# Kernel tuning notes

Measured on AMD Instinct MI355X. Metric: run time of the kernel, lower is better.

The kernel has to match this reference:

```python
import jax, jax.numpy as jnp
import numpy as np

N, D_IN, WID, LAT, DPD, H, N_SEG = 131072, 128, 512, 512, 128, 8, 256


def cumulative_segment_mean(data, segment_ids):
    # prefix mean that resets at each new (sorted) segment id
    n = data.shape[0]
    idx = jnp.arange(n)
    seg_start = jnp.concatenate([jnp.ones((1,), bool), segment_ids[1:] != segment_ids[:-1]])
    # index of the first element of each token's segment
    start_idx = jax.lax.associative_scan(jnp.maximum, jnp.where(seg_start, idx, 0))
    cs = jnp.cumsum(data, axis=0)
    base = jnp.where((start_idx > 0)[:, None], cs[jnp.maximum(start_idx - 1, 0)], jnp.zeros((), data.dtype))
    count = (idx - start_idx + 1).astype(data.dtype)[:, None]
    return (cs - base) / count


def setup_inputs() -> dict:
    key = jax.random.key(0)
    ks = jax.random.split(key, 12)
    he = lambda k, sh: jax.random.normal(k, sh, jnp.float32) * np.sqrt(2.0 / sh[0]).astype(np.float32)
    inputs = jax.random.normal(ks[0], (N, D_IN), jnp.float32)
    segment_ids = jnp.sort(jax.random.randint(ks[1], (N,), 0, N_SEG, dtype=jnp.int64))
    return {
        "inputs": inputs,
        "segment_ids": segment_ids,
        "W1": he(ks[2], (D_IN, WID)), "b1": jnp.zeros((WID,), jnp.float32),
        "W2": he(ks[3], (WID, WID)), "b2": jnp.zeros((WID,), jnp.float32),
        "W3": he(ks[4], (WID, LAT)), "b3": jnp.zeros((LAT,), jnp.float32),
        "Wr": he(ks[5], (LAT, LAT)), "br": jnp.zeros((LAT,), jnp.float32),
        "W_k": he(ks[6], (LAT + D_IN, DPD * H)),
        "W_q": jax.random.normal(ks[7], (H, DPD), jnp.float32) * 0.05,
    }


def reference(inputs, segment_ids, W1, b1, W2, b2, W3, b3, Wr, br, W_k, W_q):
    relu = jax.nn.relu
    h = relu(inputs @ W1 + b1)          # psi layer 1
    h = relu(h @ W2 + b2)               # psi layer 2
    encoded = relu(h @ W3 + b3)         # psi latent projection
    agg = cumulative_segment_mean(encoded, segment_ids)
    agg = relu(agg @ Wr + br)           # rho
    combined = jnp.concatenate([inputs, agg], axis=-1)   # [N, D_IN+LAT]
    keys = (combined @ W_k).reshape(inputs.shape[0], H, DPD)  # split+stack heads
    preattn = jnp.einsum('nhd,hd->nh', keys, W_q) / jnp.sqrt(jnp.float32(DPD))
    return preattn
```

## Files before the change

kernel.cpp:

```cpp
#include <hip/hip_runtime.h>
#include <hip/hip_bf16.h>
#include <stdint.h>

typedef unsigned short ushortT;
typedef __bf16 bf16x8 __attribute__((ext_vector_type(8)));
typedef float f32x4 __attribute__((ext_vector_type(4)));

#define N_TOK 131072
#define NSEG  256
#define RSPL  8

__device__ __forceinline__ uint32_t f2bf(float f) {
  union { float f; uint32_t u; } c; c.f = f;
  uint32_t u = c.u;
  u += 0x7fffu + ((u >> 16) & 1u);
  return u >> 16;
}
__device__ __forceinline__ float bf2f(uint32_t b) {
  union { uint32_t u; float f; } c; c.u = b << 16;
  return c.f;
}

__device__ __forceinline__ void gload_lds16(const void* g, void* l) {
  __builtin_amdgcn_global_load_lds(
      (const __attribute__((address_space(1))) void*)g,
      (__attribute__((address_space(3))) void*)l, 16, 0, 0);
}


__global__ void transpose_bf16_kernel(const float* __restrict__ W, ushortT* __restrict__ WT,
                                      int Kd, int Nd) {
  int i = blockIdx.x * 256 + threadIdx.x;
  if (i < Kd * Nd) {
    int n = i / Kd, k = i % Kd;
    WT[i] = (ushortT)f2bf(W[(size_t)k * Nd + n]);
  }
}

__global__ void weff_kernel(const float* __restrict__ Wk, const float* __restrict__ Wq,
                            ushortT* __restrict__ weffT) {
  const int c = blockIdx.x;
  const int lane = threadIdx.x;
  const float rs = 0.08838834764831845f;
#pragma unroll
  for (int h = 0; h < 8; ++h) {
    float acc = Wk[(size_t)c * 1024 + h * 128 + lane] * Wq[h * 128 + lane]
              + Wk[(size_t)c * 1024 + h * 128 + 64 + lane] * Wq[h * 128 + 64 + lane];
#pragma unroll
    for (int off = 32; off >= 1; off >>= 1) acc += __shfl_xor(acc, off, 64);
    if (lane == 0) {
      weffT[h * 640 + c]       = (ushortT)f2bf(acc * rs);
      weffT[(h + 8) * 640 + c] = 0;
    }
  }
}

__global__ void seg_bounds_kernel(const int* __restrict__ seg, int* __restrict__ gbnd) {
  const int s = (int)threadIdx.x + (int)blockIdx.x * 512;
  if (s > NSEG) return;
  int lo = 0, hi = N_TOK;
  while (lo < hi) { int m = (lo + hi) >> 1; if (seg[m] < s) lo = m + 1; else hi = m; }
  gbnd[s] = lo;
}


template <int K, bool RELU, bool BIAS, bool XF32>
__global__ __launch_bounds__(256, 2)
void gemm_m97_kernel(const void* __restrict__ Av, const ushortT* __restrict__ BT,
                     const float* __restrict__ bias, ushortT* __restrict__ C) {
  __shared__ ushortT lA[128 * 64];
  __shared__ ushortT lB[128 * 64];
  constexpr int NT = K / 64;

  const int nwg  = (int)gridDim.x;
  const int cpx  = nwg >> 3;
  const int flat = (int)blockIdx.x;
  const int swz  = (flat & 7) * cpx + (flat >> 3);
  const int bm   = swz >> 2;
  const int bn   = swz & 3;

  const int t = (int)threadIdx.x;
  const int w = t >> 6, lane = t & 63;
  const int wm = w >> 1, wn = w & 1;
  const int q = lane >> 4, lr = lane & 15;

  const int srow = t >> 3;
  const int slc  = (t & 7) ^ (srow & 7);

  const ushortT* Ab = nullptr;
  const float*   Xf = nullptr;
  if (XF32) Xf = (const float*)Av + (size_t)(bm * 128 + srow) * 128 + slc * 8;
  else      Ab = (const ushortT*)Av + (size_t)(bm * 128 + srow) * K + slc * 8;
  const ushortT* Bg = BT + (size_t)(bn * 128 + srow) * K + slc * 8;

  f32x4 acc[4][4];
#pragma unroll
  for (int i = 0; i < 4; ++i)
#pragma unroll
    for (int j = 0; j < 4; ++j) acc[i][j] = 0.f;

  const int cc0 = (q ^ (lr & 7)) << 4;
  const int cc1 = ((4 + q) ^ (lr & 7)) << 4;
  const char* lAc = (const char*)lA;
  const char* lBc = (const char*)lB;

#pragma unroll 1
  for (int kt = 0; kt < NT; ++kt) {
    if (XF32) {
      const float* src = Xf + kt * 64;
#pragma unroll
      for (int j = 0; j < 4; ++j) {
        const float4 v0 = *(const float4*)(src + (size_t)j * 32 * 128);
        const float4 v1 = *(const float4*)(src + (size_t)j * 32 * 128 + 4);
        uint4 pk;
        pk.x = f2bf(v0.x) | (f2bf(v0.y) << 16);
        pk.y = f2bf(v0.z) | (f2bf(v0.w) << 16);
        pk.z = f2bf(v1.x) | (f2bf(v1.y) << 16);
        pk.w = f2bf(v1.z) | (f2bf(v1.w) << 16);
        *(uint4*)((char*)lA + j * 4096 + t * 16) = pk;
      }
    } else {
      const ushortT* src = Ab + kt * 64;
#pragma unroll
      for (int j = 0; j < 4; ++j)
        gload_lds16(src + (size_t)j * 32 * K, (char*)lA + j * 4096 + t * 16);
    }
    {
      const ushortT* src = Bg + kt * 64;
#pragma unroll
      for (int j = 0; j < 4; ++j)
        gload_lds16(src + (size_t)j * 32 * K, (char*)lB + j * 4096 + t * 16);
    }
    __syncthreads();

    bf16x8 a0[4], a1[4], b0[4], b1[4];
#pragma unroll
    for (int m = 0; m < 4; ++m) {
      const int ro = (wm * 64 + m * 16 + lr) * 128;
      a0[m] = *(const bf16x8*)(lAc + ro + cc0);
      a1[m] = *(const bf16x8*)(lAc + ro + cc1);
    }
#pragma unroll
    for (int n = 0; n < 4; ++n) {
      const int ro = (wn * 64 + n * 16 + lr) * 128;
      b0[n] = *(const bf16x8*)(lBc + ro + cc0);
      b1[n] = *(const bf16x8*)(lBc + ro + cc1);
    }

    __builtin_amdgcn_s_setprio(1);
#pragma unroll
    for (int n = 0; n < 4; ++n)
#pragma unroll
      for (int m = 0; m < 4; ++m)
        acc[m][n] = __builtin_amdgcn_mfma_f32_16x16x32_bf16(a0[m], b0[n], acc[m][n], 0, 0, 0);
#pragma unroll
    for (int n = 0; n < 4; ++n)
#pragma unroll
      for (int m = 0; m < 4; ++m)
        acc[m][n] = __builtin_amdgcn_mfma_f32_16x16x32_bf16(a1[m], b1[n], acc[m][n], 0, 0, 0);
    __builtin_amdgcn_s_setprio(0);

    __syncthreads();
  }

  const int row0 = bm * 128 + wm * 64 + q * 4;
  const int col0 = bn * 128 + wn * 64 + lr;
#pragma unroll
  for (int n = 0; n < 4; ++n) {
    const int col = col0 + n * 16;
    const float bvv = BIAS ? bias[col] : 0.f;
#pragma unroll
    for (int m = 0; m < 4; ++m) {
#pragma unroll
      for (int r = 0; r < 4; ++r) {
        float v = acc[m][n][r] + bvv;
        if (RELU) v = fmaxf(v, 0.f);
        C[(size_t)(row0 + m * 16 + r) * 512 + col] = (ushortT)f2bf(v);
      }
    }
  }
}


__global__ __launch_bounds__(256)
void seg_sum_kernel(const ushortT* __restrict__ z, const int* __restrict__ gbnd,
                    float* __restrict__ part, int c0, int rows) {
  const int s  = (int)blockIdx.x >> 3;
  const int rg = (int)blockIdx.x & 7;
  const int t  = (int)threadIdx.x;

  const int gb0 = gbnd[s], gb1 = gbnd[s + 1];
  int beg = gb0 > c0 ? gb0 : c0;
  int end = gb1 < c0 + rows ? gb1 : c0 + rows;
  int len = end - beg; if (len < 0) len = 0;
  const int r0 = beg + ((len * rg) >> 3);
  const int r1 = beg + ((len * (rg + 1)) >> 3);

  float a0 = 0.f, a1 = 0.f;
  const uint32_t* __restrict__ zp = (const uint32_t*)z;
  int r = r0;
  for (; r + 8 <= r1; r += 8) {
    uint32_t v[8];
#pragma unroll
    for (int i = 0; i < 8; ++i) v[i] = zp[(size_t)(r + i - c0) * 256 + t];
#pragma unroll
    for (int i = 0; i < 8; ++i) { a0 += bf2f(v[i] & 0xffffu); a1 += bf2f(v[i] >> 16); }
  }
  for (; r < r1; ++r) {
    const uint32_t v = zp[(size_t)(r - c0) * 256 + t];
    a0 += bf2f(v & 0xffffu); a1 += bf2f(v >> 16);
  }
  float2 pv; pv.x = a0; pv.y = a1;
  ((float2*)part)[(s * 8 + rg) * 256 + t] = pv;
}

__global__ __launch_bounds__(256)
void seg_scan2_kernel(const ushortT* __restrict__ z, ushortT* __restrict__ gout,
                      const int* __restrict__ gbnd, const float* __restrict__ br,
                      const float* __restrict__ part,
                      const float* __restrict__ cin, float* __restrict__ cout,
                      int c0, int rows) {
  const int s  = (int)blockIdx.x >> 3;
  const int rg = (int)blockIdx.x & 7;
  const int t  = (int)threadIdx.x;

  const int gb0 = gbnd[s], gb1 = gbnd[s + 1];
  int beg = gb0 > c0 ? gb0 : c0;
  int end = gb1 < c0 + rows ? gb1 : c0 + rows;
  int len = end - beg; if (len < 0) len = 0;
  const int r0 = beg + ((len * rg) >> 3);
  const int r1 = beg + ((len * (rg + 1)) >> 3);

  const float2 cv = ((const float2*)cin)[s * 256 + t];
  float a0 = cv.x, a1 = cv.y;
  for (int q2 = 0; q2 < rg; ++q2) {
    const float2 pv = ((const float2*)part)[(s * 8 + q2) * 256 + t];
    a0 += pv.x; a1 += pv.y;
  }
  int cb = c0 - gb0; if (cb < 0) cb = 0;
  const int seglen = gb1 - gb0; if (cb > seglen) cb = seglen;
  const int cnt0 = cb + (r0 - beg);

  const float b0 = br[2 * t], b1v = br[2 * t + 1];
  const uint32_t* __restrict__ zp = (const uint32_t*)z;
  uint32_t* __restrict__ gp = (uint32_t*)gout;

  int r = r0;
  for (; r + 8 <= r1; r += 8) {
    uint32_t v[8];
#pragma unroll
    for (int i = 0; i < 8; ++i) v[i] = zp[(size_t)(r + i - c0) * 256 + t];
#pragma unroll
    for (int i = 0; i < 8; ++i) {
      a0 += bf2f(v[i] & 0xffffu);
      a1 += bf2f(v[i] >> 16);
      const float inv = 1.0f / (float)(cnt0 + (r + i) - r0 + 1);
      const float g0 = fmaxf(fmaf(a0, inv, b0), 0.f);
      const float g1 = fmaxf(fmaf(a1, inv, b1v), 0.f);
      gp[(size_t)(r + i - c0) * 256 + t] = f2bf(g0) | (f2bf(g1) << 16);
    }
  }
  for (; r < r1; ++r) {
    const uint32_t v = zp[(size_t)(r - c0) * 256 + t];
    a0 += bf2f(v & 0xffffu);
    a1 += bf2f(v >> 16);
    const float inv = 1.0f / (float)(cnt0 + r - r0 + 1);
    const float g0 = fmaxf(fmaf(a0, inv, b0), 0.f);
    const float g1 = fmaxf(fmaf(a1, inv, b1v), 0.f);
    gp[(size_t)(r - c0) * 256 + t] = f2bf(g0) | (f2bf(g1) << 16);
  }

  if (rg == 7) {
    float2 co; co.x = a0; co.y = a1;
    ((float2*)cout)[s * 256 + t] = co;
  }
}


__global__ __launch_bounds__(256)
void final_mfma_kernel(const float* __restrict__ X, const ushortT* __restrict__ g,
                       const ushortT* __restrict__ weffT, float* __restrict__ out) {
  __shared__ char lw[16 * 1296];
  const int t = (int)threadIdx.x;

#pragma unroll
  for (int i = 0; i < 5; ++i) {
    const int idx = i * 256 + t;
    const int row = idx / 80, c = idx % 80;
    *(uint4*)(lw + row * 1296 + c * 16) =
        *(const uint4*)((const char*)weffT + row * 1280 + c * 16);
  }
  __syncthreads();

  const int wv = t >> 6, lane = t & 63;
  const int q = lane >> 4, lr = lane & 15;
  const int rbase = (int)blockIdx.x * 128 + wv * 32;

  f32x4 acc[2];
  acc[0] = 0.f; acc[1] = 0.f;

#pragma unroll
  for (int kk = 0; kk < 20; ++kk) {
    const bf16x8 b = *(const bf16x8*)(lw + lr * 1296 + kk * 64 + q * 16);
#pragma unroll
    for (int mt = 0; mt < 2; ++mt) {
      const int row = rbase + mt * 16 + lr;
      union { ushortT u[8]; bf16x8 v; } a;
      if (kk < 4) {
        const float* xr = X + (size_t)row * 128 + kk * 32 + q * 8;
        const float4 v0 = *(const float4*)xr;
        const float4 v1 = *(const float4*)(xr + 4);
        a.u[0] = (ushortT)f2bf(v0.x); a.u[1] = (ushortT)f2bf(v0.y);
        a.u[2] = (ushortT)f2bf(v0.z); a.u[3] = (ushortT)f2bf(v0.w);
        a.u[4] = (ushortT)f2bf(v1.x); a.u[5] = (ushortT)f2bf(v1.y);
        a.u[6] = (ushortT)f2bf(v1.z); a.u[7] = (ushortT)f2bf(v1.w);
      } else {
        a.v = *(const bf16x8*)(g + (size_t)row * 512 + (kk - 4) * 32 + q * 8);
      }
      acc[mt] = __builtin_amdgcn_mfma_f32_16x16x32_bf16(a.v, b, acc[mt], 0, 0, 0);
    }
  }

  if (lr < 8) {
#pragma unroll
    for (int mt = 0; mt < 2; ++mt)
#pragma unroll
      for (int r = 0; r < 4; ++r)
        out[(size_t)(rbase + mt * 16 + q * 4 + r) * 8 + lr] = acc[mt][r];
  }
}


extern "C" void kernel_launch(void* const* d_in, const int* in_sizes, int n_in,
                              void* d_out, int out_size, void* d_ws, size_t ws_size,
                              hipStream_t stream) {
  const float* X  = (const float*)d_in[0];
  const int*   sg = (const int*)d_in[1];
  const float* W1 = (const float*)d_in[2];
  const float* b1 = (const float*)d_in[3];
  const float* W2 = (const float*)d_in[4];
  const float* b2 = (const float*)d_in[5];
  const float* W3 = (const float*)d_in[6];
  const float* b3 = (const float*)d_in[7];
  const float* Wr = (const float*)d_in[8];
  const float* br = (const float*)d_in[9];
  const float* Wk = (const float*)d_in[10];
  const float* Wq = (const float*)d_in[11];
  float* out = (float*)d_out;

  const size_t szW1T  = 512 * 128 * 2;
  const size_t szWT   = 512 * 512 * 2;
  const size_t szWeff = 16 * 640 * 2;
  const size_t szPart = (size_t)NSEG * RSPL * 256 * 2 * 4;
  const size_t szCar  = (size_t)NSEG * 256 * 2 * 4;
  const size_t szBnd  = (NSEG + 1) * 4;
  const size_t fixed  = szW1T + 3 * szWT + szWeff + szPart + 2 * szCar + szBnd + 512;

  int CH = 0;
  const int cands[6] = {131072, 65536, 32768, 16384, 8192, 4096};
  for (int i = 0; i < 6; ++i) {
    const size_t need = fixed + 2 * (size_t)cands[i] * 512 * 2;
    if (need <= ws_size) { CH = cands[i]; break; }
  }
  if (CH == 0) CH = 4096;

  char* p = (char*)d_ws;
  ushortT* W1T   = (ushortT*)p; p += szW1T;
  ushortT* W2T   = (ushortT*)p; p += szWT;
  ushortT* W3T   = (ushortT*)p; p += szWT;
  ushortT* WrT   = (ushortT*)p; p += szWT;
  ushortT* weffT = (ushortT*)p; p += szWeff;
  float*   part  = (float*)p;   p += szPart;
  float*   carA  = (float*)p;   p += szCar;
  float*   carB  = (float*)p;   p += szCar;
  int*     gbnd  = (int*)p;     p += (szBnd + 255) & ~255ull;
  ushortT* p1    = (ushortT*)p; p += (size_t)CH * 512 * 2;
  ushortT* p2    = (ushortT*)p;

  transpose_bf16_kernel<<<(512 * 128 + 255) / 256, 256, 0, stream>>>(W1, W1T, 128, 512);
  transpose_bf16_kernel<<<(512 * 512 + 255) / 256, 256, 0, stream>>>(W2, W2T, 512, 512);
  transpose_bf16_kernel<<<(512 * 512 + 255) / 256, 256, 0, stream>>>(W3, W3T, 512, 512);
  transpose_bf16_kernel<<<(512 * 512 + 255) / 256, 256, 0, stream>>>(Wr, WrT, 512, 512);
  weff_kernel<<<640, 64, 0, stream>>>(Wk, Wq, weffT);
  seg_bounds_kernel<<<1, 512, 0, stream>>>(sg, gbnd);
  hipMemsetAsync(carA, 0, szCar, stream);

  int par = 0;
  for (int c0 = 0; c0 < N_TOK; c0 += CH) {
    const int gG = (CH / 128) * 4;
    float* cin  = par ? carB : carA;
    float* cout = par ? carA : carB;
    gemm_m97_kernel<128, true,  true,  true ><<<gG, 256, 0, stream>>>(X + (size_t)c0 * 128, W1T, b1, p1);
    gemm_m97_kernel<512, true,  true,  false><<<gG, 256, 0, stream>>>(p1, W2T, b2, p2);
    gemm_m97_kernel<512, true,  true,  false><<<gG, 256, 0, stream>>>(p2, W3T, b3, p1);
    gemm_m97_kernel<512, false, false, false><<<gG, 256, 0, stream>>>(p1, WrT, nullptr, p2);
    seg_sum_kernel <<<NSEG * RSPL, 256, 0, stream>>>(p2, gbnd, part, c0, CH);
    seg_scan2_kernel<<<NSEG * RSPL, 256, 0, stream>>>(p2, p1, gbnd, br, part,
                                                      cin, cout, c0, CH);
    final_mfma_kernel<<<CH / 128, 256, 0, stream>>>(X + (size_t)c0 * 128, p1, weffT,
                                                    out + (size_t)c0 * 8);
    par ^= 1;
  }
}
```

Baseline: 435.4 us.

## Add 256x256-tile 8-wave GEMM kernel for the three K=512 layers

Introduces a new GEMM kernel using 256x256 output tiles with 512 threads (8 waves), double-buffered 64KB LDS stages, swizzled LDS layout, and four barrier-separated MFMA phases with s_setprio raising around compute. It replaces the 128x128 gemm_m97 kernel for the W2, W3 and Wr layers to raise data reuse per tile and interleave LDS loads with MFMA across waves. The larger tile gives fewer workgroups and one block per CU (128KB LDS), which risks lower occupancy and poorer load balance if the chunk size yields few tiles.

```diff
diff --git a/kernel.cpp b/kernel.cpp
--- a/kernel.cpp
+++ b/kernel.cpp
@@ -61,6 +61,151 @@
   int lo = 0, hi = N_TOK;
   while (lo < hi) { int m = (lo + hi) >> 1; if (seg[m] < s) lo = m + 1; else hi = m; }
   gbnd[s] = lo;
+}
+
+
+template <int K, bool RELU, bool BIAS>
+__global__ __launch_bounds__(512, 1)
+void gemm_8ph_kernel(const ushortT* __restrict__ A, const ushortT* __restrict__ BT,
+                     const float* __restrict__ bias, ushortT* __restrict__ C) {
+  __shared__ char lds[2 * 65536];
+  constexpr int NT = K / 64;
+
+  const int nwg  = (int)gridDim.x;
+  const int cpx  = nwg >> 3;
+  const int flat = (int)blockIdx.x;
+  const int swz  = (flat & 7) * cpx + (flat >> 3);
+  const int bm   = swz >> 1;
+  const int bn   = swz & 1;
+
+  const int t = (int)threadIdx.x;
+  const int w = t >> 6, lane = t & 63;
+  const int wm = w >> 2, wn = w & 3;
+  const int q = lane >> 4, lr = lane & 15;
+
+  const int srow = t >> 3;
+  const int slc  = (t & 7) ^ (srow & 7);
+  const ushortT* Ag = A  + (size_t)(bm * 256 + srow) * K + slc * 8;
+  const ushortT* Bg = BT + (size_t)(bn * 256 + srow) * K + slc * 8;
+
+  f32x4 acc[8][4];
+#pragma unroll
+  for (int i = 0; i < 8; ++i)
+#pragma unroll
+    for (int j = 0; j < 4; ++j) acc[i][j] = 0.f;
+
+#define STAGE8(buf, tile)                                                       \
+  {                                                                             \
+    char* _d = lds + (buf) * 65536 + t * 16;                                    \
+    const ushortT* _ga = Ag + (tile) * 64;                                      \
+    _Pragma("unroll")                                                           \
+    for (int _p = 0; _p < 4; ++_p)                                              \
+      gload_lds16(_ga + (size_t)_p * 64 * K, _d + _p * 8192);                   \
+    const ushortT* _gb = Bg + (tile) * 64;                                      \
+    _Pragma("unroll")                                                           \
+    for (int _p = 0; _p < 4; ++_p)                                              \
+      gload_lds16(_gb + (size_t)_p * 64 * K, _d + 32768 + _p * 8192);           \
+  }
+
+  STAGE8(0, 0);
+  asm volatile("s_waitcnt vmcnt(0)" ::: "memory");
+  __builtin_amdgcn_s_barrier();
+  asm volatile("" ::: "memory");
+
+  const int cc0 = (q ^ (lr & 7)) << 4;
+  const int cc1 = ((4 + q) ^ (lr & 7)) << 4;
+  const int aro = (wm * 128 + lr) * 128;
+  const int bro = 32768 + (wn * 64 + lr) * 128;
+
+  int cur = 0;
+#pragma unroll 1
+  for (int j = 0; j < NT; ++j) {
+    const char* sa = lds + cur * 65536;
+    bf16x8 a[4], b[4];
+
+#pragma unroll
+    for (int n = 0; n < 4; ++n) b[n] = *(const bf16x8*)(sa + bro + n * 2048 + cc0);
+#pragma unroll
+    for (int m = 0; m < 4; ++m) a[m] = *(const bf16x8*)(sa + aro + m * 2048 + cc0);
+    if (j + 1 < NT) STAGE8(cur ^ 1, j + 1);
+    __builtin_amdgcn_s_barrier();
+    asm volatile("" ::: "memory");
+    __builtin_amdgcn_s_setprio(1);
+#pragma unroll
+    for (int n = 0; n < 4; ++n)
+#pragma unroll
+      for (int m = 0; m < 4; ++m)
+        acc[m][n] = __builtin_amdgcn_mfma_f32_16x16x32_bf16(a[m], b[n], acc[m][n], 0, 0, 0);
+    __builtin_amdgcn_s_setprio(0);
+    __builtin_amdgcn_s_barrier();
+    asm volatile("" ::: "memory");
+
+#pragma unroll
+    for (int m = 0; m < 4; ++m) a[m] = *(const bf16x8*)(sa + aro + 8192 + m * 2048 + cc0);
+    __builtin_amdgcn_s_barrier();
+    asm volatile("" ::: "memory");
+    __builtin_amdgcn_s_setprio(1);
+#pragma unroll
+    for (int n = 0; n < 4; ++n)
+#pragma unroll
+      for (int m = 0; m < 4; ++m)
+        acc[m + 4][n] = __builtin_amdgcn_mfma_f32_16x16x32_bf16(a[m], b[n], acc[m + 4][n], 0, 0, 0);
+    __builtin_amdgcn_s_setprio(0);
+    __builtin_amdgcn_s_barrier();
+    asm volatile("" ::: "memory");
+
+#pragma unroll
+    for (int n = 0; n < 4; ++n) b[n] = *(const bf16x8*)(sa + bro + n * 2048 + cc1);
+#pragma unroll
+    for (int m = 0; m < 4; ++m) a[m] = *(const bf16x8*)(sa + aro + m * 2048 + cc1);
+    __builtin_amdgcn_s_barrier();
+    asm volatile("" ::: "memory");
+    __builtin_amdgcn_s_setprio(1);
+#pragma unroll
+    for (int n = 0; n < 4; ++n)
+#pragma unroll
+      for (int m = 0; m < 4; ++m)
+        acc[m][n] = __builtin_amdgcn_mfma_f32_16x16x32_bf16(a[m], b[n], acc[m][n], 0, 0, 0);
+    __builtin_amdgcn_s_setprio(0);
+    __builtin_amdgcn_s_barrier();
+    asm volatile("" ::: "memory");
+
+#pragma unroll
+    for (int m = 0; m < 4; ++m) a[m] = *(const bf16x8*)(sa + aro + 8192 + m * 2048 + cc1);
+    __builtin_amdgcn_s_barrier();
+    asm volatile("" ::: "memory");
+    __builtin_amdgcn_s_setprio(1);
+#pragma unroll
+    for (int n = 0; n < 4; ++n)
+#pragma unroll
+      for (int m = 0; m < 4; ++m)
+        acc[m + 4][n] = __builtin_amdgcn_mfma_f32_16x16x32_bf16(a[m], b[n], acc[m + 4][n], 0, 0, 0);
+    __builtin_amdgcn_s_setprio(0);
+    if (j + 1 < NT)
+      asm volatile("s_waitcnt vmcnt(0)" ::: "memory");
+    __builtin_amdgcn_s_barrier();
+    asm volatile("" ::: "memory");
+
+    cur ^= 1;
+  }
+#undef STAGE8
+
+  const int row0 = bm * 256 + wm * 128 + q * 4;
+  const int col0 = bn * 256 + wn * 64 + lr;
+#pragma unroll
+  for (int n = 0; n < 4; ++n) {
+    const int col = col0 + n * 16;
+    const float bvv = BIAS ? bias[col] : 0.f;
+#pragma unroll
+    for (int m = 0; m < 8; ++m) {
+#pragma unroll
+      for (int r = 0; r < 4; ++r) {
+        float v = acc[m][n][r] + bvv;
+        if (RELU) v = fmaxf(v, 0.f);
+        C[(size_t)(row0 + m * 16 + r) * 512 + col] = (ushortT)f2bf(v);
+      }
+    }
+  }
 }
 
 
@@ -387,13 +532,14 @@
 
   int par = 0;
   for (int c0 = 0; c0 < N_TOK; c0 += CH) {
-    const int gG = (CH / 128) * 4;
+    const int gG1 = (CH / 128) * 4;
+    const int gG8 = (CH / 256) * 2;
     float* cin  = par ? carB : carA;
     float* cout = par ? carA : carB;
-    gemm_m97_kernel<128, true,  true,  true ><<<gG, 256, 0, stream>>>(X + (size_t)c0 * 128, W1T, b1, p1);
-    gemm_m97_kernel<512, true,  true,  false><<<gG, 256, 0, stream>>>(p1, W2T, b2, p2);
-    gemm_m97_kernel<512, true,  true,  false><<<gG, 256, 0, stream>>>(p2, W3T, b3, p1);
-    gemm_m97_kernel<512, false, false, false><<<gG, 256, 0, stream>>>(p1, WrT, nullptr, p2);
+    gemm_m97_kernel<128, true, true, true><<<gG1, 256, 0, stream>>>(X + (size_t)c0 * 128, W1T, b1, p1);
+    gemm_8ph_kernel<512, true,  true ><<<gG8, 512, 0, stream>>>(p1, W2T, b2, p2);
+    gemm_8ph_kernel<512, true,  true ><<<gG8, 512, 0, stream>>>(p2, W3T, b3, p1);
+    gemm_8ph_kernel<512, false, false><<<gG8, 512, 0, stream>>>(p1, WrT, nullptr, p2);
     seg_sum_kernel <<<NSEG * RSPL, 256, 0, stream>>>(p2, gbnd, part, c0, CH);
     seg_scan2_kernel<<<NSEG * RSPL, 256, 0, stream>>>(p2, p1, gbnd, br, part,
                                                       cin, cout, c0, CH);
```

After: 508.1 us. 16.7% more time.
